# Kernel tuning notes

Hardware: AMD Instinct MI355X
Metric: run time of the kernel (lower is better)

The kernel has to match this reference:

```python
import jax, jax.numpy as jnp
import numpy as np

Q, L = 512, 4096


def setup_inputs() -> dict:
    key = jax.random.key(0)
    ks = jax.random.split(key, 12)
    def rn(k, shape, s=0.05):
        return jax.random.normal(k, shape, jnp.float32) * s
    return {
        "reactions": jax.random.normal(ks[0], (1, Q, 256), jnp.float32),
        "protein":   jax.random.normal(ks[1], (1, L, 1024), jnp.float32),
        # conv1d(1024->256, k=1) == pointwise linear
        "Wc":  rn(ks[2], (256, 1024)), "bc":  jnp.zeros((256,), jnp.float32),
        "W1":  rn(ks[3], (64, 256)),   "b1":  jnp.zeros((64,), jnp.float32),
        "W2":  rn(ks[4], (64, 256)),   "b2":  jnp.zeros((64,), jnp.float32),
        "Wa":  rn(ks[5], (64, 64)),    "ba":  jnp.zeros((64,), jnp.float32),
        "Wpa": rn(ks[6], (64, 64)),    "bpa": jnp.zeros((64,), jnp.float32),
        "Wra": rn(ks[7], (64, 64)),    "bra": jnp.zeros((64,), jnp.float32),
        "Wf1": rn(ks[8], (256, 128)),  "bf1": jnp.zeros((256,), jnp.float32),
        "Wf2": rn(ks[9], (128, 256)),  "bf2": jnp.zeros((128,), jnp.float32),
        "Wf3": rn(ks[10], (1, 128)),   "bf3": jnp.zeros((1,), jnp.float32),
    }


def reference(reactions, protein, Wc, bc, W1, b1, W2, b2, Wa, ba,
              Wpa, bpa, Wra, bra, Wf1, bf1, Wf2, bf2, Wf3, bf3):
    # protein: [1, L, 1024] -> 1x1 conv over channels == linear -> [L, 256]
    p = jax.nn.relu(protein[0] @ Wc.T + bc)
    # reactions: [1, Q, 256] -> [Q, 64]
    r = jax.nn.relu(reactions[0] @ W2.T + b2)
    # protein tokens -> [L, 64]
    k = jax.nn.relu(p @ W1.T + b1)

    ra = r @ Wra.T + bra            # [Q, 64]
    pa = k @ Wpa.T + bpa            # [L, 64]
    # broadcast outer-sum + relu + small linear: [Q, L, 64]
    A = jax.nn.relu(ra[:, None, :] + pa[None, :, :]) @ Wa.T + ba

    r_gate = jax.nn.sigmoid(jnp.mean(A, axis=1))   # [Q, 64]
    p_gate = jax.nn.sigmoid(jnp.mean(A, axis=0))   # [L, 64]

    rxnfp = r + r * r_gate                          # [Q, 64]
    prot = jnp.max(k + k * p_gate, axis=0)          # [64]  maxpool over L

    ctx = jnp.concatenate(
        [rxnfp, jnp.broadcast_to(prot, (rxnfp.shape[0], 64))], axis=1)  # [Q,128]

    # dropout layers are identity in eval mode
    h = jax.nn.leaky_relu(ctx @ Wf1.T + bf1)
    h = jax.nn.leaky_relu(h @ Wf2.T + bf2)
    out = h @ Wf3.T + bf3
    return out.reshape(-1)                          # [Q]
```

## Files before the change

kernel.cpp:

```cpp
#include <hip/hip_runtime.h>
#include <hip/hip_bf16.h>
#include <math.h>

#define TPB 256

typedef __attribute__((ext_vector_type(8))) short s16x8;
typedef __attribute__((ext_vector_type(4))) float f32x4;

#define MFMA16(a, b, c) __builtin_amdgcn_mfma_f32_16x16x32_bf16((a), (b), (c), 0, 0, 0)

constexpr unsigned OFF_P    = 0u;
constexpr unsigned OFF_K    = OFF_P    + 4096u*256u;
constexpr unsigned OFF_PA   = OFF_K    + 4096u*64u;
constexpr unsigned OFF_R    = OFF_PA   + 4096u*64u;
constexpr unsigned OFF_RA   = OFF_R    + 512u*64u;
constexpr unsigned OFF_SR   = OFF_RA   + 512u*64u;
constexpr unsigned OFF_PMAX = OFF_SR   + 512u*64u;
constexpr unsigned OFF_SP   = OFF_PMAX + 64u;
constexpr unsigned OFF_PAT  = OFF_SP   + 4096u*64u;
constexpr unsigned OFF_RAT  = OFF_PAT  + 64u*4096u;

__device__ __forceinline__ short f2bf(float x) {
  union { float f; unsigned u; } v; v.f = x;
  unsigned r = v.u + 0x7FFFu + ((v.u >> 16) & 1u);
  return (short)(r >> 16);
}
__device__ __forceinline__ unsigned pkbf(float a, float b) {
  __hip_bfloat162 h = __float22bfloat162_rn(make_float2(a, b));
  union { __hip_bfloat162 h2; unsigned u; } v; v.h2 = h;
  return v.u;
}
union U8 { s16x8 s; unsigned u[4]; };

__global__ __launch_bounds__(TPB, 2) void k1_gemm(
    const float* __restrict__ prot, const float* __restrict__ Wc,
    const float* __restrict__ bc,   float* __restrict__ ws)
{
  int bid = blockIdx.x;
  int tid = threadIdx.x;
  if (bid >= 512) {
    if (tid < 16)
      *(float4*)&ws[OFF_PMAX + tid * 4] = make_float4(0.f, 0.f, 0.f, 0.f);
    return;
  }

  __shared__ __align__(16) short Asm[32 * 72];
  __shared__ __align__(16) short Bsm[64 * 72];

  int m0 = (bid >> 2) * 32;
  int n0 = (bid & 3) * 64;
  int wave = tid >> 6, lane = tid & 63;
  int wm = (wave & 1) * 16, wn = (wave >> 1) * 32;
  int lm = lane & 15, quad = lane >> 4;

  int arow = tid >> 3, aseg = (tid & 7) * 8;
  int brow = tid >> 2, bseg = (tid & 3) * 16;

  const float* Ag = prot + (size_t)(m0 + arow) * 1024 + aseg;
  const float* Bg = Wc   + (size_t)(n0 + brow) * 1024 + bseg;

  float4 a4[2], b4[4];
#pragma unroll
  for (int i = 0; i < 2; ++i) a4[i] = *(const float4*)(Ag + i * 4);
#pragma unroll
  for (int i = 0; i < 4; ++i) b4[i] = *(const float4*)(Bg + i * 4);

  f32x4 acc[2] = {};

  for (int kc = 0; kc < 16; ++kc) {
    __syncthreads();
    {
      U8 s;
      s.u[0] = pkbf(a4[0].x, a4[0].y); s.u[1] = pkbf(a4[0].z, a4[0].w);
      s.u[2] = pkbf(a4[1].x, a4[1].y); s.u[3] = pkbf(a4[1].z, a4[1].w);
      *(s16x8*)&Asm[arow * 72 + aseg] = s.s;
    }
#pragma unroll
    for (int h = 0; h < 2; ++h) {
      U8 s;
      s.u[0] = pkbf(b4[h*2].x,   b4[h*2].y);
      s.u[1] = pkbf(b4[h*2].z,   b4[h*2].w);
      s.u[2] = pkbf(b4[h*2+1].x, b4[h*2+1].y);
      s.u[3] = pkbf(b4[h*2+1].z, b4[h*2+1].w);
      *(s16x8*)&Bsm[brow * 72 + bseg + h * 8] = s.s;
    }
    if (kc < 15) {
#pragma unroll
      for (int i = 0; i < 2; ++i) a4[i] = *(const float4*)(Ag + (kc + 1) * 64 + i * 4);
#pragma unroll
      for (int i = 0; i < 4; ++i) b4[i] = *(const float4*)(Bg + (kc + 1) * 64 + i * 4);
    }
    __syncthreads();
#pragma unroll
    for (int ks = 0; ks < 2; ++ks) {
      s16x8 af = *(const s16x8*)&Asm[(wm + lm) * 72 + ks * 32 + quad * 8];
#pragma unroll
      for (int ni = 0; ni < 2; ++ni) {
        s16x8 bfv = *(const s16x8*)&Bsm[(wn + ni * 16 + lm) * 72 + ks * 32 + quad * 8];
        acc[ni] = MFMA16(af, bfv, acc[ni]);
      }
    }
  }

#pragma unroll
  for (int ni = 0; ni < 2; ++ni) {
    int col = n0 + wn + ni * 16 + lm;
    float bcv = bc[col];
#pragma unroll
    for (int r = 0; r < 4; ++r) {
      int row = m0 + wm + quad * 4 + r;
      ws[OFF_P + (unsigned)row * 256u + col] = fmaxf(acc[ni][r] + bcv, 0.f);
    }
  }
}

__global__ __launch_bounds__(TPB, 2) void k2_heads(
    const float* __restrict__ reactions,
    const float* __restrict__ W1,  const float* __restrict__ b1,
    const float* __restrict__ W2,  const float* __restrict__ b2,
    const float* __restrict__ Wpa, const float* __restrict__ bpa,
    const float* __restrict__ Wra, const float* __restrict__ bra,
    float* __restrict__ ws)
{
  __shared__ __align__(16) short Asm[32 * 264];
  __shared__ __align__(16) short Bsm[64 * 264];
  __shared__ __align__(16) short Ksm[32 * 72];
  __shared__ __align__(16) short Wsm[64 * 72];
  int bid = blockIdx.x, tid = threadIdx.x;
  bool isProt = bid < 128;
  int row0 = (isProt ? bid : (bid - 128)) * 32;
  const float* src  = isProt ? (ws + OFF_P) : reactions;
  const float* Wst1 = isProt ? W1 : W2;
  const float* bv   = isProt ? b1 : b2;
  const float* Wst2 = isProt ? Wpa : Wra;
  const float* b2nd = isProt ? bpa : bra;
  float* out1  = ws + (isProt ? OFF_K : OFF_R);
  float* out2  = ws + (isProt ? OFF_PA : OFF_RA);
  float* out2T = ws + (isProt ? OFF_PAT : OFF_RAT);
  unsigned tstride = isProt ? 4096u : 512u;

  {
    int row = tid >> 3, seg = (tid & 7) * 32;
    const float* sp = src + (size_t)(row0 + row) * 256 + seg;
    float4 f[8];
#pragma unroll
    for (int i = 0; i < 8; ++i) f[i] = *(const float4*)(sp + i * 4);
#pragma unroll
    for (int i = 0; i < 4; ++i) {
      U8 s;
      s.u[0] = pkbf(f[2*i].x,   f[2*i].y);
      s.u[1] = pkbf(f[2*i].z,   f[2*i].w);
      s.u[2] = pkbf(f[2*i+1].x, f[2*i+1].y);
      s.u[3] = pkbf(f[2*i+1].z, f[2*i+1].w);
      *(s16x8*)&Asm[row * 264 + seg + i * 8] = s.s;
    }
  }
  {
    int row = tid >> 2, seg = (tid & 3) * 64;
    const float* sp = Wst1 + (size_t)row * 256 + seg;
#pragma unroll
    for (int i = 0; i < 8; ++i) {
      float4 fa = *(const float4*)(sp + i * 8);
      float4 fb = *(const float4*)(sp + i * 8 + 4);
      U8 s;
      s.u[0] = pkbf(fa.x, fa.y); s.u[1] = pkbf(fa.z, fa.w);
      s.u[2] = pkbf(fb.x, fb.y); s.u[3] = pkbf(fb.z, fb.w);
      *(s16x8*)&Bsm[row * 264 + seg + i * 8] = s.s;
    }
  }
  {
    int row = tid >> 2, seg = (tid & 3) * 16;
    const float* sp = Wst2 + (size_t)row * 64 + seg;
#pragma unroll
    for (int i = 0; i < 2; ++i) {
      float4 fa = *(const float4*)(sp + i * 8);
      float4 fb = *(const float4*)(sp + i * 8 + 4);
      U8 s;
      s.u[0] = pkbf(fa.x, fa.y); s.u[1] = pkbf(fa.z, fa.w);
      s.u[2] = pkbf(fb.x, fb.y); s.u[3] = pkbf(fb.z, fb.w);
      *(s16x8*)&Wsm[row * 72 + seg + i * 8] = s.s;
    }
  }
  __syncthreads();

  int wave = tid >> 6, lane = tid & 63;
  int lm = lane & 15, quad = lane >> 4;
  int wm = (wave >> 1) * 16, wn = (wave & 1) * 32;

  f32x4 acc[2] = {};
#pragma unroll
  for (int kc = 0; kc < 8; ++kc) {
    s16x8 a = *(const s16x8*)&Asm[(wm + lm) * 264 + kc * 32 + quad * 8];
#pragma unroll
    for (int ni = 0; ni < 2; ++ni) {
      s16x8 b = *(const s16x8*)&Bsm[(wn + ni * 16 + lm) * 264 + kc * 32 + quad * 8];
      acc[ni] = MFMA16(a, b, acc[ni]);
    }
  }
#pragma unroll
  for (int ni = 0; ni < 2; ++ni) {
    int col = wn + ni * 16 + lm;
    float bb = bv[col];
#pragma unroll
    for (int r = 0; r < 4; ++r) {
      int row = wm + quad * 4 + r;
      float kv = fmaxf(acc[ni][r] + bb, 0.f);
      out1[(size_t)(row0 + row) * 64 + col] = kv;
      Ksm[row * 72 + col] = f2bf(kv);
    }
  }
  __syncthreads();

  f32x4 acc2[2] = {};
#pragma unroll
  for (int kc = 0; kc < 2; ++kc) {
    s16x8 a = *(const s16x8*)&Ksm[(wm + lm) * 72 + kc * 32 + quad * 8];
#pragma unroll
    for (int ni = 0; ni < 2; ++ni) {
      s16x8 b = *(const s16x8*)&Wsm[(wn + ni * 16 + lm) * 72 + kc * 32 + quad * 8];
      acc2[ni] = MFMA16(a, b, acc2[ni]);
    }
  }
#pragma unroll
  for (int ni = 0; ni < 2; ++ni) {
    int col = wn + ni * 16 + lm;
    float bb = b2nd[col];
#pragma unroll
    for (int r = 0; r < 4; ++r) {
      int row = wm + quad * 4 + r;
      float v = acc2[ni][r] + bb;
      out2[(size_t)(row0 + row) * 64 + col] = v;
      out2T[(size_t)col * tstride + (row0 + row)] = v;
    }
  }
}

__global__ __launch_bounds__(TPB) void k3h_hist(float* __restrict__ ws)
{
  __shared__ float xcol[4096];
  __shared__ float rcol[512];
  __shared__ float hc[1025];
  __shared__ float hs[1025];
  __shared__ float rmn[4], rmx[4];
  int bid = blockIdx.x, tid = threadIdx.x;
  int wave = tid >> 6, lane = tid & 63;
  bool passA = bid < 64;
  int c = passA ? bid : (bid - 64);
  const float* paT = ws + OFF_PAT + (size_t)c * 4096;
  const float* raT = ws + OFF_RAT + (size_t)c * 512;

  for (int i = tid * 4; i < 4096; i += TPB * 4)
    *(float4*)&xcol[i] = *(const float4*)(paT + i);
  if (tid * 4 < 512)
    *(float4*)&rcol[tid * 4] = *(const float4*)(raT + tid * 4);
  for (int i = tid; i < 1025; i += TPB) { hc[i] = 0.f; hs[i] = 0.f; }
  __syncthreads();

  const float* hsrc = passA ? xcol : rcol;
  int hn = passA ? 4096 : 512;
  float mn = 1e30f, mx = -1e30f;
  for (int i = tid; i < hn; i += TPB) {
    float x = hsrc[i];
    mn = fminf(mn, x); mx = fmaxf(mx, x);
  }
#pragma unroll
  for (int off = 32; off > 0; off >>= 1) {
    mn = fminf(mn, __shfl_down(mn, off));
    mx = fmaxf(mx, __shfl_down(mx, off));
  }
  if (lane == 0) { rmn[wave] = mn; rmx[wave] = mx; }
  __syncthreads();
  mn = fminf(fminf(rmn[0], rmn[1]), fminf(rmn[2], rmn[3]));
  mx = fmaxf(fmaxf(rmx[0], rmx[1]), fmaxf(rmx[2], rmx[3]));
  float w = (mx - mn) * (1.f / 1024.f);
  float invw = (w > 1e-30f) ? 1.f / w : 0.f;
  for (int i = tid; i < hn; i += TPB) {
    float x = hsrc[i];
    int b = (int)((x - mn) * invw);
    b = b < 0 ? 0 : (b > 1023 ? 1023 : b);
    atomicAdd(&hc[b], 1.f);
    atomicAdd(&hs[b], x);
  }
  __syncthreads();
  if (wave == 0) {
    float vc[16], vs[16], sc = 0.f, ss = 0.f;
#pragma unroll
    for (int i = 0; i < 16; ++i) {
      vc[i] = hc[lane * 16 + i]; sc += vc[i];
      vs[i] = hs[lane * 16 + i]; ss += vs[i];
    }
    float tc = sc, ts = ss;
#pragma unroll
    for (int off = 1; off < 64; off <<= 1) {
      float oc = __shfl_down(tc, off);
      float os = __shfl_down(ts, off);
      if (lane + off < 64) { tc += oc; ts += os; }
    }
    float runc = tc - sc, runs = ts - ss;
#pragma unroll
    for (int i = 15; i >= 0; --i) {
      runc += vc[i]; hc[lane * 16 + i] = runc;
      runs += vs[i]; hs[lane * 16 + i] = runs;
    }
  }
  __syncthreads();

  if (passA) {
    for (int q = tid; q < 512; q += TPB) {
      float u = rcol[q];
      float thr = -u;
      int b;
      if (thr < mn) b = 0;
      else { b = (int)((thr - mn) * invw) + 1; b = b > 1024 ? 1024 : b; }
      ws[OFF_SR + (unsigned)q * 64u + c] = u * hc[b] + hs[b];
    }
  } else {
    for (int l = tid; l < 4096; l += TPB) {
      float v = xcol[l];
      float thr = -v;
      int b;
      if (thr < mn) b = 0;
      else { b = (int)((thr - mn) * invw) + 1; b = b > 1024 ? 1024 : b; }
      ws[OFF_SP + (unsigned)l * 64u + c] = v * hc[b] + hs[b];
    }
  }
}

__global__ __launch_bounds__(TPB) void k3b_gate(
    const float* __restrict__ Wa, const float* __restrict__ ba,
    float* __restrict__ ws)
{
  __shared__ float sp[16 * 64];
  __shared__ float wat[64 * 65];
  int bid = blockIdx.x, tid = threadIdx.x;
  int c = tid & 63, g = tid >> 6;
  int l0 = bid * 16;
  {
    int idx = tid * 4;
    float4 v = *(const float4*)&ws[OFF_SP + (unsigned)l0 * 64u + idx];
    v.x *= (1.f / 512.f); v.y *= (1.f / 512.f);
    v.z *= (1.f / 512.f); v.w *= (1.f / 512.f);
    *(float4*)&sp[idx] = v;
  }
  for (int it = 0; it < 16; ++it) {
    int idx = it * TPB + tid;
    wat[(idx & 63) * 65 + (idx >> 6)] = Wa[idx];
  }
  __syncthreads();
  float vmax = 0.f;
  float bac = ba[c];
#pragma unroll
  for (int i = 0; i < 4; ++i) {
    int ll = g * 4 + i;
    float dot = 0.f;
#pragma unroll 8
    for (int jj = 0; jj < 64; ++jj)
      dot += sp[ll * 64 + jj] * wat[jj * 65 + c];
    float pg = 1.f / (1.f + __expf(-(dot + bac)));
    float val = ws[OFF_K + (unsigned)(l0 + ll) * 64u + c] * (1.f + pg);
    vmax = fmaxf(vmax, val);
  }
  atomicMax((int*)&ws[OFF_PMAX + c], __float_as_int(vmax));
}

__global__ __launch_bounds__(TPB) void k4_final(
    const float* __restrict__ Wa,  const float* __restrict__ ba,
    const float* __restrict__ Wf1, const float* __restrict__ bf1,
    const float* __restrict__ Wf2, const float* __restrict__ bf2,
    const float* __restrict__ Wf3, const float* __restrict__ bf3,
    float* __restrict__ ws, float* __restrict__ out)
{
  __shared__ __align__(16) short mrb[16 * 72];
  __shared__ __align__(16) short wab[64 * 72];
  __shared__ __align__(16) short ctxb[16 * 136];
  __shared__ __align__(16) short h1b[16 * 264];
  __shared__ __align__(16) short wgt[256 * 136];
  __shared__ float red[64];
  int bid = blockIdx.x, tid = threadIdx.x;
  int q0 = bid * 16;
  int wave = tid >> 6, lane = tid & 63;
  int lm = lane & 15, quad = lane >> 4;

  {
    int q = tid >> 4, c4 = (tid & 15) * 4;
    float4 v = *(const float4*)&ws[OFF_SR + (unsigned)(q0 + q) * 64u + c4];
    uint2 st = make_uint2(pkbf(v.x * (1.f/4096.f), v.y * (1.f/4096.f)),
                          pkbf(v.z * (1.f/4096.f), v.w * (1.f/4096.f)));
    *(uint2*)&mrb[q * 72 + c4] = st;
  }
#pragma unroll
  for (int it = 0; it < 4; ++it) {
    int i4 = it * TPB + tid;
    int row = i4 >> 4, c4 = (i4 & 15) * 4;
    float4 v = *(const float4*)&Wa[row * 64 + c4];
    uint2 st = make_uint2(pkbf(v.x, v.y), pkbf(v.z, v.w));
    *(uint2*)&wab[row * 72 + c4] = st;
  }
  __syncthreads();

  f32x4 gacc = {};
#pragma unroll
  for (int kc = 0; kc < 2; ++kc) {
    s16x8 a = *(const s16x8*)&mrb[lm * 72 + kc * 32 + quad * 8];
    s16x8 b = *(const s16x8*)&wab[(wave * 16 + lm) * 72 + kc * 32 + quad * 8];
    gacc = MFMA16(a, b, gacc);
  }
  {
    int c = wave * 16 + lm;
    float bac = ba[c];
    short pb = f2bf(ws[OFF_PMAX + c]);
#pragma unroll
    for (int r = 0; r < 4; ++r) {
      int q = quad * 4 + r;
      float gg = 1.f / (1.f + __expf(-(gacc[r] + bac)));
      float rv = ws[OFF_R + (unsigned)(q0 + q) * 64u + c];
      ctxb[q * 136 + c]      = f2bf(rv * (1.f + gg));
      ctxb[q * 136 + 64 + c] = pb;
    }
  }
#pragma unroll 4
  for (int it = 0; it < 32; ++it) {
    int i4 = it * TPB + tid;
    int row = i4 >> 5, c4 = (i4 & 31) * 4;
    float4 v = *(const float4*)&Wf1[row * 128 + c4];
    uint2 st = make_uint2(pkbf(v.x, v.y), pkbf(v.z, v.w));
    *(uint2*)&wgt[row * 136 + c4] = st;
  }
  __syncthreads();

  f32x4 h[4] = {};
#pragma unroll
  for (int kc = 0; kc < 4; ++kc) {
    s16x8 a = *(const s16x8*)&ctxb[lm * 136 + kc * 32 + quad * 8];
#pragma unroll
    for (int nt = 0; nt < 4; ++nt) {
      s16x8 b = *(const s16x8*)&wgt[(wave * 64 + nt * 16 + lm) * 136 + kc * 32 + quad * 8];
      h[nt] = MFMA16(a, b, h[nt]);
    }
  }
#pragma unroll
  for (int nt = 0; nt < 4; ++nt) {
    int n = wave * 64 + nt * 16 + lm;
    float bb = bf1[n];
#pragma unroll
    for (int r = 0; r < 4; ++r) {
      int q = quad * 4 + r;
      float v = h[nt][r] + bb;
      v = v > 0.f ? v : 0.01f * v;
      h1b[q * 264 + n] = f2bf(v);
    }
  }
  __syncthreads();

#pragma unroll 4
  for (int it = 0; it < 32; ++it) {
    int i4 = it * TPB + tid;
    int row = i4 >> 6, c4 = (i4 & 63) * 4;
    float4 v = *(const float4*)&Wf2[row * 256 + c4];
    uint2 st = make_uint2(pkbf(v.x, v.y), pkbf(v.z, v.w));
    *(uint2*)&wgt[row * 264 + c4] = st;
  }
  __syncthreads();

  f32x4 o[2] = {};
#pragma unroll
  for (int kc = 0; kc < 8; ++kc) {
    s16x8 a = *(const s16x8*)&h1b[lm * 264 + kc * 32 + quad * 8];
#pragma unroll
    for (int nt = 0; nt < 2; ++nt) {
      s16x8 b = *(const s16x8*)&wgt[(wave * 32 + nt * 16 + lm) * 264 + kc * 32 + quad * 8];
      o[nt] = MFMA16(a, b, o[nt]);
    }
  }
  float pv[4] = {0.f, 0.f, 0.f, 0.f};
#pragma unroll
  for (int nt = 0; nt < 2; ++nt) {
    int m = wave * 32 + nt * 16 + lm;
    float bb = bf2[m], w3 = Wf3[m];
#pragma unroll
    for (int r = 0; r < 4; ++r) {
      float v = o[nt][r] + bb;
      v = v > 0.f ? v : 0.01f * v;
      pv[r] += v * w3;
    }
  }
#pragma unroll
  for (int msk = 1; msk < 16; msk <<= 1)
#pragma unroll
    for (int r = 0; r < 4; ++r) pv[r] += __shfl_xor(pv[r], msk);
  if (lm == 0) {
#pragma unroll
    for (int r = 0; r < 4; ++r) red[(quad * 4 + r) * 4 + wave] = pv[r];
  }
  __syncthreads();
  if (tid < 16)
    out[q0 + tid] = red[tid * 4] + red[tid * 4 + 1] + red[tid * 4 + 2] +
                    red[tid * 4 + 3] + bf3[0];
}

extern "C" void kernel_launch(void* const* d_in, const int* in_sizes, int n_in,
                              void* d_out, int out_size, void* d_ws, size_t ws_size,
                              hipStream_t stream)
{
  const float* reactions = (const float*)d_in[0];
  const float* protein   = (const float*)d_in[1];
  const float* Wc  = (const float*)d_in[2];
  const float* bc  = (const float*)d_in[3];
  const float* W1  = (const float*)d_in[4];
  const float* b1  = (const float*)d_in[5];
  const float* W2  = (const float*)d_in[6];
  const float* b2  = (const float*)d_in[7];
  const float* Wa  = (const float*)d_in[8];
  const float* ba  = (const float*)d_in[9];
  const float* Wpa = (const float*)d_in[10];
  const float* bpa = (const float*)d_in[11];
  const float* Wra = (const float*)d_in[12];
  const float* bra = (const float*)d_in[13];
  const float* Wf1 = (const float*)d_in[14];
  const float* bf1 = (const float*)d_in[15];
  const float* Wf2 = (const float*)d_in[16];
  const float* bf2 = (const float*)d_in[17];
  const float* Wf3 = (const float*)d_in[18];
  const float* bf3 = (const float*)d_in[19];
  float* ws  = (float*)d_ws;
  float* out = (float*)d_out;

  hipLaunchKernelGGL(k1_gemm, dim3(513), dim3(TPB), 0, stream,
                     protein, Wc, bc, ws);
  hipLaunchKernelGGL(k2_heads, dim3(144), dim3(TPB), 0, stream,
                     reactions, W1, b1, W2, b2, Wpa, bpa, Wra, bra, ws);
  hipLaunchKernelGGL(k3h_hist, dim3(128), dim3(TPB), 0, stream, ws);
  hipLaunchKernelGGL(k3b_gate, dim3(256), dim3(TPB), 0, stream, Wa, ba, ws);
  hipLaunchKernelGGL(k4_final, dim3(32), dim3(TPB), 0, stream,
                     Wa, ba, Wf1, bf1, Wf2, bf2, Wf3, bf3, ws, out);
}
```

Baseline: 170.0 us.

## Fuse histogram, gate and final MLP kernels into one cooperative kernel

Merges the three tail kernels (histogram prefix sums, protein gate with max-pool, and final MLP) into a single cooperative launch that uses grid.sync between phases. The PMAX zeroing moves from an extra GEMM block into the fused kernel. The goal is to remove two kernel launch gaps and drain bubbles. In exchange the kernel needs 94KB of static shared memory and occupancy 1, and it pays the cost of grid-wide barriers.

```diff
diff --git a/kernel.cpp b/kernel.cpp
--- a/kernel.cpp
+++ b/kernel.cpp
@@ -1,8 +1,10 @@
 #include <hip/hip_runtime.h>
+#include <hip/hip_cooperative_groups.h>
 #include <hip/hip_bf16.h>
 #include <math.h>
 
 #define TPB 256
+namespace cg = cooperative_groups;
 
 typedef __attribute__((ext_vector_type(8))) short s16x8;
 typedef __attribute__((ext_vector_type(4))) float f32x4;
@@ -38,11 +40,6 @@
 {
   int bid = blockIdx.x;
   int tid = threadIdx.x;
-  if (bid >= 512) {
-    if (tid < 16)
-      *(float4*)&ws[OFF_PMAX + tid * 4] = make_float4(0.f, 0.f, 0.f, 0.f);
-    return;
-  }
 
   __shared__ __align__(16) short Asm[32 * 72];
   __shared__ __align__(16) short Bsm[64 * 72];
@@ -235,267 +232,277 @@
   }
 }
 
-__global__ __launch_bounds__(TPB) void k3h_hist(float* __restrict__ ws)
-{
-  __shared__ float xcol[4096];
-  __shared__ float rcol[512];
-  __shared__ float hc[1025];
-  __shared__ float hs[1025];
-  __shared__ float rmn[4], rmx[4];
-  int bid = blockIdx.x, tid = threadIdx.x;
-  int wave = tid >> 6, lane = tid & 63;
-  bool passA = bid < 64;
-  int c = passA ? bid : (bid - 64);
-  const float* paT = ws + OFF_PAT + (size_t)c * 4096;
-  const float* raT = ws + OFF_RAT + (size_t)c * 512;
-
-  for (int i = tid * 4; i < 4096; i += TPB * 4)
-    *(float4*)&xcol[i] = *(const float4*)(paT + i);
-  if (tid * 4 < 512)
-    *(float4*)&rcol[tid * 4] = *(const float4*)(raT + tid * 4);
-  for (int i = tid; i < 1025; i += TPB) { hc[i] = 0.f; hs[i] = 0.f; }
-  __syncthreads();
-
-  const float* hsrc = passA ? xcol : rcol;
-  int hn = passA ? 4096 : 512;
-  float mn = 1e30f, mx = -1e30f;
-  for (int i = tid; i < hn; i += TPB) {
-    float x = hsrc[i];
-    mn = fminf(mn, x); mx = fmaxf(mx, x);
-  }
-#pragma unroll
-  for (int off = 32; off > 0; off >>= 1) {
-    mn = fminf(mn, __shfl_down(mn, off));
-    mx = fmaxf(mx, __shfl_down(mx, off));
-  }
-  if (lane == 0) { rmn[wave] = mn; rmx[wave] = mx; }
-  __syncthreads();
-  mn = fminf(fminf(rmn[0], rmn[1]), fminf(rmn[2], rmn[3]));
-  mx = fmaxf(fmaxf(rmx[0], rmx[1]), fmaxf(rmx[2], rmx[3]));
-  float w = (mx - mn) * (1.f / 1024.f);
-  float invw = (w > 1e-30f) ? 1.f / w : 0.f;
-  for (int i = tid; i < hn; i += TPB) {
-    float x = hsrc[i];
-    int b = (int)((x - mn) * invw);
-    b = b < 0 ? 0 : (b > 1023 ? 1023 : b);
-    atomicAdd(&hc[b], 1.f);
-    atomicAdd(&hs[b], x);
-  }
-  __syncthreads();
-  if (wave == 0) {
-    float vc[16], vs[16], sc = 0.f, ss = 0.f;
-#pragma unroll
-    for (int i = 0; i < 16; ++i) {
-      vc[i] = hc[lane * 16 + i]; sc += vc[i];
-      vs[i] = hs[lane * 16 + i]; ss += vs[i];
-    }
-    float tc = sc, ts = ss;
-#pragma unroll
-    for (int off = 1; off < 64; off <<= 1) {
-      float oc = __shfl_down(tc, off);
-      float os = __shfl_down(ts, off);
-      if (lane + off < 64) { tc += oc; ts += os; }
-    }
-    float runc = tc - sc, runs = ts - ss;
-#pragma unroll
-    for (int i = 15; i >= 0; --i) {
-      runc += vc[i]; hc[lane * 16 + i] = runc;
-      runs += vs[i]; hs[lane * 16 + i] = runs;
-    }
-  }
-  __syncthreads();
-
-  if (passA) {
-    for (int q = tid; q < 512; q += TPB) {
-      float u = rcol[q];
-      float thr = -u;
-      int b;
-      if (thr < mn) b = 0;
-      else { b = (int)((thr - mn) * invw) + 1; b = b > 1024 ? 1024 : b; }
-      ws[OFF_SR + (unsigned)q * 64u + c] = u * hc[b] + hs[b];
-    }
-  } else {
-    for (int l = tid; l < 4096; l += TPB) {
-      float v = xcol[l];
-      float thr = -v;
-      int b;
-      if (thr < mn) b = 0;
-      else { b = (int)((thr - mn) * invw) + 1; b = b > 1024 ? 1024 : b; }
-      ws[OFF_SP + (unsigned)l * 64u + c] = v * hc[b] + hs[b];
-    }
-  }
-}
-
-__global__ __launch_bounds__(TPB) void k3b_gate(
-    const float* __restrict__ Wa, const float* __restrict__ ba,
-    float* __restrict__ ws)
-{
-  __shared__ float sp[16 * 64];
-  __shared__ float wat[64 * 65];
-  int bid = blockIdx.x, tid = threadIdx.x;
-  int c = tid & 63, g = tid >> 6;
-  int l0 = bid * 16;
-  {
-    int idx = tid * 4;
-    float4 v = *(const float4*)&ws[OFF_SP + (unsigned)l0 * 64u + idx];
-    v.x *= (1.f / 512.f); v.y *= (1.f / 512.f);
-    v.z *= (1.f / 512.f); v.w *= (1.f / 512.f);
-    *(float4*)&sp[idx] = v;
-  }
-  for (int it = 0; it < 16; ++it) {
-    int idx = it * TPB + tid;
-    wat[(idx & 63) * 65 + (idx >> 6)] = Wa[idx];
-  }
-  __syncthreads();
-  float vmax = 0.f;
-  float bac = ba[c];
-#pragma unroll
-  for (int i = 0; i < 4; ++i) {
-    int ll = g * 4 + i;
-    float dot = 0.f;
-#pragma unroll 8
-    for (int jj = 0; jj < 64; ++jj)
-      dot += sp[ll * 64 + jj] * wat[jj * 65 + c];
-    float pg = 1.f / (1.f + __expf(-(dot + bac)));
-    float val = ws[OFF_K + (unsigned)(l0 + ll) * 64u + c] * (1.f + pg);
-    vmax = fmaxf(vmax, val);
-  }
-  atomicMax((int*)&ws[OFF_PMAX + c], __float_as_int(vmax));
-}
-
-__global__ __launch_bounds__(TPB) void k4_final(
+__global__ __launch_bounds__(TPB, 1) void k3_mega(
     const float* __restrict__ Wa,  const float* __restrict__ ba,
     const float* __restrict__ Wf1, const float* __restrict__ bf1,
     const float* __restrict__ Wf2, const float* __restrict__ bf2,
     const float* __restrict__ Wf3, const float* __restrict__ bf3,
     float* __restrict__ ws, float* __restrict__ out)
 {
-  __shared__ __align__(16) short mrb[16 * 72];
-  __shared__ __align__(16) short wab[64 * 72];
-  __shared__ __align__(16) short ctxb[16 * 136];
-  __shared__ __align__(16) short h1b[16 * 264];
-  __shared__ __align__(16) short wgt[256 * 136];
-  __shared__ float red[64];
+  __shared__ __align__(16) char smem[94208];
+  cg::grid_group grid = cg::this_grid();
   int bid = blockIdx.x, tid = threadIdx.x;
-  int q0 = bid * 16;
   int wave = tid >> 6, lane = tid & 63;
-  int lm = lane & 15, quad = lane >> 4;
+
+  if (bid < 128) {
+    float* xcol = (float*)smem;
+    float* rcol = xcol + 4096;
+    float* hc   = rcol + 512;
+    float* hs   = hc + 1025;
+    float* rmn  = hs + 1025;
+    float* rmx  = rmn + 4;
+    bool passA = bid < 64;
+    int c = passA ? bid : (bid - 64);
+    const float* paT = ws + OFF_PAT + (size_t)c * 4096;
+    const float* raT = ws + OFF_RAT + (size_t)c * 512;
+
+    for (int i = tid * 4; i < 4096; i += TPB * 4)
+      *(float4*)&xcol[i] = *(const float4*)(paT + i);
+    if (tid * 4 < 512)
+      *(float4*)&rcol[tid * 4] = *(const float4*)(raT + tid * 4);
+    for (int i = tid; i < 1025; i += TPB) { hc[i] = 0.f; hs[i] = 0.f; }
+    __syncthreads();
+
+    const float* hsrc = passA ? xcol : rcol;
+    int hn = passA ? 4096 : 512;
+    float mn = 1e30f, mx = -1e30f;
+    for (int i = tid; i < hn; i += TPB) {
+      float x = hsrc[i];
+      mn = fminf(mn, x); mx = fmaxf(mx, x);
+    }
+#pragma unroll
+    for (int off = 32; off > 0; off >>= 1) {
+      mn = fminf(mn, __shfl_down(mn, off));
+      mx = fmaxf(mx, __shfl_down(mx, off));
+    }
+    if (lane == 0) { rmn[wave] = mn; rmx[wave] = mx; }
+    __syncthreads();
+    mn = fminf(fminf(rmn[0], rmn[1]), fminf(rmn[2], rmn[3]));
+    mx = fmaxf(fmaxf(rmx[0], rmx[1]), fmaxf(rmx[2], rmx[3]));
+    float w = (mx - mn) * (1.f / 1024.f);
+    float invw = (w > 1e-30f) ? 1.f / w : 0.f;
+    for (int i = tid; i < hn; i += TPB) {
+      float x = hsrc[i];
+      int b = (int)((x - mn) * invw);
+      b = b < 0 ? 0 : (b > 1023 ? 1023 : b);
+      atomicAdd(&hc[b], 1.f);
+      atomicAdd(&hs[b], x);
+    }
+    __syncthreads();
+    if (wave == 0) {
+      float vc[16], vs[16], sc = 0.f, ss = 0.f;
+#pragma unroll
+      for (int i = 0; i < 16; ++i) {
+        vc[i] = hc[lane * 16 + i]; sc += vc[i];
+        vs[i] = hs[lane * 16 + i]; ss += vs[i];
+      }
+      float tc = sc, ts = ss;
+#pragma unroll
+      for (int off = 1; off < 64; off <<= 1) {
+        float oc = __shfl_down(tc, off);
+        float os = __shfl_down(ts, off);
+        if (lane + off < 64) { tc += oc; ts += os; }
+      }
+      float runc = tc - sc, runs = ts - ss;
+#pragma unroll
+      for (int i = 15; i >= 0; --i) {
+        runc += vc[i]; hc[lane * 16 + i] = runc;
+        runs += vs[i]; hs[lane * 16 + i] = runs;
+      }
+    }
+    __syncthreads();
+
+    if (passA) {
+      for (int q = tid; q < 512; q += TPB) {
+        float u = rcol[q];
+        float thr = -u;
+        int b;
+        if (thr < mn) b = 0;
+        else { b = (int)((thr - mn) * invw) + 1; b = b > 1024 ? 1024 : b; }
+        ws[OFF_SR + (unsigned)q * 64u + c] = u * hc[b] + hs[b];
+      }
+    } else {
+      for (int l = tid; l < 4096; l += TPB) {
+        float v = xcol[l];
+        float thr = -v;
+        int b;
+        if (thr < mn) b = 0;
+        else { b = (int)((thr - mn) * invw) + 1; b = b > 1024 ? 1024 : b; }
+        ws[OFF_SP + (unsigned)l * 64u + c] = v * hc[b] + hs[b];
+      }
+    }
+  } else if (bid == 128) {
+    if (tid < 16)
+      *(float4*)&ws[OFF_PMAX + tid * 4] = make_float4(0.f, 0.f, 0.f, 0.f);
+  }
+  __threadfence();
+  grid.sync();
+  __threadfence();
 
   {
-    int q = tid >> 4, c4 = (tid & 15) * 4;
-    float4 v = *(const float4*)&ws[OFF_SR + (unsigned)(q0 + q) * 64u + c4];
-    uint2 st = make_uint2(pkbf(v.x * (1.f/4096.f), v.y * (1.f/4096.f)),
-                          pkbf(v.z * (1.f/4096.f), v.w * (1.f/4096.f)));
-    *(uint2*)&mrb[q * 72 + c4] = st;
-  }
-#pragma unroll
-  for (int it = 0; it < 4; ++it) {
-    int i4 = it * TPB + tid;
-    int row = i4 >> 4, c4 = (i4 & 15) * 4;
-    float4 v = *(const float4*)&Wa[row * 64 + c4];
-    uint2 st = make_uint2(pkbf(v.x, v.y), pkbf(v.z, v.w));
-    *(uint2*)&wab[row * 72 + c4] = st;
-  }
-  __syncthreads();
-
-  f32x4 gacc = {};
-#pragma unroll
-  for (int kc = 0; kc < 2; ++kc) {
-    s16x8 a = *(const s16x8*)&mrb[lm * 72 + kc * 32 + quad * 8];
-    s16x8 b = *(const s16x8*)&wab[(wave * 16 + lm) * 72 + kc * 32 + quad * 8];
-    gacc = MFMA16(a, b, gacc);
-  }
-  {
-    int c = wave * 16 + lm;
+    float* sp  = (float*)smem;
+    float* wat = sp + 1024;
+    int c = tid & 63, g = tid >> 6;
+    int l0 = bid * 16;
+    {
+      int idx = tid * 4;
+      float4 v = *(const float4*)&ws[OFF_SP + (unsigned)l0 * 64u + idx];
+      v.x *= (1.f / 512.f); v.y *= (1.f / 512.f);
+      v.z *= (1.f / 512.f); v.w *= (1.f / 512.f);
+      *(float4*)&sp[idx] = v;
+    }
+    for (int it = 0; it < 16; ++it) {
+      int idx = it * TPB + tid;
+      wat[(idx & 63) * 65 + (idx >> 6)] = Wa[idx];
+    }
+    __syncthreads();
+    float vmax = 0.f;
     float bac = ba[c];
-    short pb = f2bf(ws[OFF_PMAX + c]);
-#pragma unroll
-    for (int r = 0; r < 4; ++r) {
-      int q = quad * 4 + r;
-      float gg = 1.f / (1.f + __expf(-(gacc[r] + bac)));
-      float rv = ws[OFF_R + (unsigned)(q0 + q) * 64u + c];
-      ctxb[q * 136 + c]      = f2bf(rv * (1.f + gg));
-      ctxb[q * 136 + 64 + c] = pb;
-    }
-  }
+#pragma unroll
+    for (int i = 0; i < 4; ++i) {
+      int ll = g * 4 + i;
+      float dot = 0.f;
+#pragma unroll 8
+      for (int jj = 0; jj < 64; ++jj)
+        dot += sp[ll * 64 + jj] * wat[jj * 65 + c];
+      float pg = 1.f / (1.f + __expf(-(dot + bac)));
+      float val = ws[OFF_K + (unsigned)(l0 + ll) * 64u + c] * (1.f + pg);
+      vmax = fmaxf(vmax, val);
+    }
+    atomicMax((int*)&ws[OFF_PMAX + c], __float_as_int(vmax));
+    __syncthreads();
+  }
+  __threadfence();
+  grid.sync();
+  __threadfence();
+
+  if (bid < 32) {
+    short* mrb  = (short*)smem;
+    short* wab  = mrb + 1152;
+    short* ctxb = wab + 4608;
+    short* h1b  = ctxb + 2176;
+    short* wgt  = h1b + 4224;
+    float* red  = (float*)(wgt + 34816);
+    int q0 = bid * 16;
+    int lm = lane & 15, quad = lane >> 4;
+
+    {
+      int q = tid >> 4, c4 = (tid & 15) * 4;
+      float4 v = *(const float4*)&ws[OFF_SR + (unsigned)(q0 + q) * 64u + c4];
+      uint2 st = make_uint2(pkbf(v.x * (1.f/4096.f), v.y * (1.f/4096.f)),
+                            pkbf(v.z * (1.f/4096.f), v.w * (1.f/4096.f)));
+      *(uint2*)&mrb[q * 72 + c4] = st;
+    }
+#pragma unroll
+    for (int it = 0; it < 4; ++it) {
+      int i4 = it * TPB + tid;
+      int row = i4 >> 4, c4 = (i4 & 15) * 4;
+      float4 v = *(const float4*)&Wa[row * 64 + c4];
+      uint2 st = make_uint2(pkbf(v.x, v.y), pkbf(v.z, v.w));
+      *(uint2*)&wab[row * 72 + c4] = st;
+    }
+    __syncthreads();
+
+    f32x4 gacc = {};
+#pragma unroll
+    for (int kc = 0; kc < 2; ++kc) {
+      s16x8 a = *(const s16x8*)&mrb[lm * 72 + kc * 32 + quad * 8];
+      s16x8 b = *(const s16x8*)&wab[(wave * 16 + lm) * 72 + kc * 32 + quad * 8];
+      gacc = MFMA16(a, b, gacc);
+    }
+    {
+      int c = wave * 16 + lm;
+      float bac = ba[c];
+      unsigned pmu = atomicOr((unsigned*)&ws[OFF_PMAX + c], 0u);
+      short pb = f2bf(__uint_as_float(pmu));
+#pragma unroll
+      for (int r = 0; r < 4; ++r) {
+        int q = quad * 4 + r;
+        float gg = 1.f / (1.f + __expf(-(gacc[r] + bac)));
+        float rv = ws[OFF_R + (unsigned)(q0 + q) * 64u + c];
+        ctxb[q * 136 + c]      = f2bf(rv * (1.f + gg));
+        ctxb[q * 136 + 64 + c] = pb;
+      }
+    }
 #pragma unroll 4
-  for (int it = 0; it < 32; ++it) {
-    int i4 = it * TPB + tid;
-    int row = i4 >> 5, c4 = (i4 & 31) * 4;
-    float4 v = *(const float4*)&Wf1[row * 128 + c4];
-    uint2 st = make_uint2(pkbf(v.x, v.y), pkbf(v.z, v.w));
-    *(uint2*)&wgt[row * 136 + c4] = st;
-  }
-  __syncthreads();
-
-  f32x4 h[4] = {};
-#pragma unroll
-  for (int kc = 0; kc < 4; ++kc) {
-    s16x8 a = *(const s16x8*)&ctxb[lm * 136 + kc * 32 + quad * 8];
+    for (int it = 0; it < 32; ++it) {
+      int i4 = it * TPB + tid;
+      int row = i4 >> 5, c4 = (i4 & 31) * 4;
+      float4 v = *(const float4*)&Wf1[row * 128 + c4];
+      uint2 st = make_uint2(pkbf(v.x, v.y), pkbf(v.z, v.w));
+      *(uint2*)&wgt[row * 136 + c4] = st;
+    }
+    __syncthreads();
+
+    f32x4 h[4] = {};
+#pragma unroll
+    for (int kc = 0; kc < 4; ++kc) {
+      s16x8 a = *(const s16x8*)&ctxb[lm * 136 + kc * 32 + quad * 8];
+#pragma unroll
+      for (int nt = 0; nt < 4; ++nt) {
+        s16x8 b = *(const s16x8*)&wgt[(wave * 64 + nt * 16 + lm) * 136 + kc * 32 + quad * 8];
+        h[nt] = MFMA16(a, b, h[nt]);
+      }
+    }
 #pragma unroll
     for (int nt = 0; nt < 4; ++nt) {
-      s16x8 b = *(const s16x8*)&wgt[(wave * 64 + nt * 16 + lm) * 136 + kc * 32 + quad * 8];
-      h[nt] = MFMA16(a, b, h[nt]);
-    }
-  }
-#pragma unroll
-  for (int nt = 0; nt < 4; ++nt) {
-    int n = wave * 64 + nt * 16 + lm;
-    float bb = bf1[n];
-#pragma unroll
-    for (int r = 0; r < 4; ++r) {
-      int q = quad * 4 + r;
-      float v = h[nt][r] + bb;
-      v = v > 0.f ? v : 0.01f * v;
-      h1b[q * 264 + n] = f2bf(v);
-    }
-  }
-  __syncthreads();
+      int n = wave * 64 + nt * 16 + lm;
+      float bb = bf1[n];
+#pragma unroll
+      for (int r = 0; r < 4; ++r) {
+        int q = quad * 4 + r;
+        float v = h[nt][r] + bb;
+        v = v > 0.f ? v : 0.01f * v;
+        h1b[q * 264 + n] = f2bf(v);
+      }
+    }
+    __syncthreads();
 
 #pragma unroll 4
-  for (int it = 0; it < 32; ++it) {
-    int i4 = it * TPB + tid;
-    int row = i4 >> 6, c4 = (i4 & 63) * 4;
-    float4 v = *(const float4*)&Wf2[row * 256 + c4];
-    uint2 st = make_uint2(pkbf(v.x, v.y), pkbf(v.z, v.w));
-    *(uint2*)&wgt[row * 264 + c4] = st;
-  }
-  __syncthreads();
-
-  f32x4 o[2] = {};
-#pragma unroll
-  for (int kc = 0; kc < 8; ++kc) {
-    s16x8 a = *(const s16x8*)&h1b[lm * 264 + kc * 32 + quad * 8];
+    for (int it = 0; it < 32; ++it) {
+      int i4 = it * TPB + tid;
+      int row = i4 >> 6, c4 = (i4 & 63) * 4;
+      float4 v = *(const float4*)&Wf2[row * 256 + c4];
+      uint2 st = make_uint2(pkbf(v.x, v.y), pkbf(v.z, v.w));
+      *(uint2*)&wgt[row * 264 + c4] = st;
+    }
+    __syncthreads();
+
+    f32x4 o[2] = {};
+#pragma unroll
+    for (int kc = 0; kc < 8; ++kc) {
+      s16x8 a = *(const s16x8*)&h1b[lm * 264 + kc * 32 + quad * 8];
+#pragma unroll
+      for (int nt = 0; nt < 2; ++nt) {
+        s16x8 b = *(const s16x8*)&wgt[(wave * 32 + nt * 16 + lm) * 264 + kc * 32 + quad * 8];
+        o[nt] = MFMA16(a, b, o[nt]);
+      }
+    }
+    float pv[4] = {0.f, 0.f, 0.f, 0.f};
 #pragma unroll
     for (int nt = 0; nt < 2; ++nt) {
-      s16x8 b = *(const s16x8*)&wgt[(wave * 32 + nt * 16 + lm) * 264 + kc * 32 + quad * 8];
-      o[nt] = MFMA16(a, b, o[nt]);
-    }
-  }
-  float pv[4] = {0.f, 0.f, 0.f, 0.f};
-#pragma unroll
-  for (int nt = 0; nt < 2; ++nt) {
-    int m = wave * 32 + nt * 16 + lm;
-    float bb = bf2[m], w3 = Wf3[m];
-#pragma unroll
-    for (int r = 0; r < 4; ++r) {
-      float v = o[nt][r] + bb;
-      v = v > 0.f ? v : 0.01f * v;
-      pv[r] += v * w3;
-    }
-  }
-#pragma unroll
-  for (int msk = 1; msk < 16; msk <<= 1)
-#pragma unroll
-    for (int r = 0; r < 4; ++r) pv[r] += __shfl_xor(pv[r], msk);
-  if (lm == 0) {
-#pragma unroll
-    for (int r = 0; r < 4; ++r) red[(quad * 4 + r) * 4 + wave] = pv[r];
-  }
-  __syncthreads();
-  if (tid < 16)
-    out[q0 + tid] = red[tid * 4] + red[tid * 4 + 1] + red[tid * 4 + 2] +
-                    red[tid * 4 + 3] + bf3[0];
+      int m = wave * 32 + nt * 16 + lm;
+      float bb = bf2[m], w3 = Wf3[m];
+#pragma unroll
+      for (int r = 0; r < 4; ++r) {
+        float v = o[nt][r] + bb;
+        v = v > 0.f ? v : 0.01f * v;
+        pv[r] += v * w3;
+      }
+    }
+#pragma unroll
+    for (int msk = 1; msk < 16; msk <<= 1)
+#pragma unroll
+      for (int r = 0; r < 4; ++r) pv[r] += __shfl_xor(pv[r], msk);
+    if (lm == 0) {
+#pragma unroll
+      for (int r = 0; r < 4; ++r) red[(quad * 4 + r) * 4 + wave] = pv[r];
+    }
+    __syncthreads();
+    if (tid < 16)
+      out[q0 + tid] = red[tid * 4] + red[tid * 4 + 1] + red[tid * 4 + 2] +
+                      red[tid * 4 + 3] + bf3[0];
+  }
 }
 
 extern "C" void kernel_launch(void* const* d_in, const int* in_sizes, int n_in,
@@ -525,12 +532,18 @@
   float* ws  = (float*)d_ws;
   float* out = (float*)d_out;
 
-  hipLaunchKernelGGL(k1_gemm, dim3(513), dim3(TPB), 0, stream,
+  hipLaunchKernelGGL(k1_gemm, dim3(512), dim3(TPB), 0, stream,
                      protein, Wc, bc, ws);
   hipLaunchKernelGGL(k2_heads, dim3(144), dim3(TPB), 0, stream,
                      reactions, W1, b1, W2, b2, Wpa, bpa, Wra, bra, ws);
-  hipLaunchKernelGGL(k3h_hist, dim3(128), dim3(TPB), 0, stream, ws);
-  hipLaunchKernelGGL(k3b_gate, dim3(256), dim3(TPB), 0, stream, Wa, ba, ws);
-  hipLaunchKernelGGL(k4_final, dim3(32), dim3(TPB), 0, stream,
-                     Wa, ba, Wf1, bf1, Wf2, bf2, Wf3, bf3, ws, out);
+
+  const float* a_Wa = Wa;  const float* a_ba = ba;
+  const float* a_Wf1 = Wf1; const float* a_bf1 = bf1;
+  const float* a_Wf2 = Wf2; const float* a_bf2 = bf2;
+  const float* a_Wf3 = Wf3; const float* a_bf3 = bf3;
+  float* a_ws = ws; float* a_out = out;
+  void* args[10] = {&a_Wa, &a_ba, &a_Wf1, &a_bf1, &a_Wf2, &a_bf2,
+                    &a_Wf3, &a_bf3, &a_ws, &a_out};
+  hipLaunchCooperativeKernel((void*)k3_mega, dim3(256), dim3(TPB),
+                             args, 0, stream);
 }
```

Result: slower. 324.4 us (+90.8%).
